# Kernel optimization log

Hardware: AMD Instinct MI355X
Metric: run time of the kernel (lower is better)

Reference implementation:

```python
import jax, jax.numpy as jnp
import numpy as np

D_MODEL = 1024
D_STATE = 16
D_CONV = 4
EXPAND = 2
D_INNER = D_MODEL * EXPAND
BATCH = 4
SEQLEN = 4096


def setup_inputs() -> dict:
    key = jax.random.key(0)
    ks = jax.random.split(key, 10)
    s = 1.0 / np.sqrt(D_MODEL)
    si = 1.0 / np.sqrt(D_INNER)
    return {
        "x": jax.random.normal(ks[0], (BATCH, SEQLEN, D_MODEL), jnp.float32),
        "x_proj_w": jax.random.normal(ks[1], (D_INNER, D_MODEL), jnp.float32) * s,
        "dt_proj_w": jax.random.normal(ks[2], (D_INNER, D_MODEL), jnp.float32) * s,
        "dt_proj_b": jax.random.normal(ks[3], (D_INNER,), jnp.float32) * 0.1,
        "A_log": jax.random.normal(ks[4], (D_INNER, D_STATE), jnp.float32),
        "D": jnp.ones((D_INNER,), jnp.float32),
        "B_proj_w": jax.random.normal(ks[5], (D_STATE, D_MODEL), jnp.float32) * s,
        "C_proj_w": jax.random.normal(ks[6], (D_STATE, D_MODEL), jnp.float32) * s,
        "conv_w": jax.random.normal(ks[7], (D_INNER, 1, D_CONV), jnp.float32) * 0.5,
        "conv_b": jax.random.normal(ks[8], (D_INNER,), jnp.float32) * 0.1,
        "out_proj_w": jax.random.normal(ks[9], (D_MODEL, D_INNER), jnp.float32) * si,
    }


def _selective_scan(xc, delta, A, B, C, D):
    # xc, delta: (b, L, d_inner); B, C: (b, L, d_state); A: (d_inner, d_state)
    batch, seqlen, d_inner = xc.shape
    d_state = A.shape[1]

    def step(h, inp):
        x_t, dt, B_t, C_t = inp  # (b,di), (b,di), (b,ds), (b,ds)
        A_disc = jnp.exp(dt[:, :, None] * A[None])           # (b, di, ds)
        h = A_disc * h + (dt[:, :, None] * B_t[:, None, :]) * x_t[:, :, None]
        y_t = jnp.einsum('bds,bs->bd', h, C_t) + D[None, :] * x_t
        return h, y_t

    h0 = jnp.zeros((batch, d_inner, d_state), xc.dtype)
    xs = (jnp.swapaxes(xc, 0, 1), jnp.swapaxes(delta, 0, 1),
          jnp.swapaxes(B, 0, 1), jnp.swapaxes(C, 0, 1))
    _, ys = jax.lax.scan(step, h0, xs)  # ys: (L, b, d_inner)
    return jnp.swapaxes(ys, 0, 1)


def reference(x, x_proj_w, dt_proj_w, dt_proj_b, A_log, D, B_proj_w, C_proj_w, conv_w, conv_b, out_proj_w):
    seqlen = x.shape[1]
    x_inner = x @ x_proj_w.T  # (b, L, d_inner)
    # causal depthwise conv1d: torch pads both sides by d_conv-1 then keeps first L,
    # equivalent to left-pad (d_conv-1, 0)
    xc = jax.lax.conv_general_dilated(
        jnp.swapaxes(x_inner, 1, 2), conv_w,
        window_strides=(1,), padding=[(D_CONV - 1, 0)],
        dimension_numbers=('NCH', 'OIH', 'NCH'),
        feature_group_count=D_INNER)
    xc = jnp.swapaxes(xc + conv_b[None, :, None], 1, 2)
    xc = jax.nn.silu(xc)
    B = x @ B_proj_w.T
    C = x @ C_proj_w.T
    delta = jax.nn.softplus(x @ dt_proj_w.T + dt_proj_b)
    A = -jnp.exp(A_log.astype(jnp.float32))
    y = _selective_scan(xc, delta, A, B, C, D)
    return y @ out_proj_w.T
```

## Files before the change

### kernel.cpp

```cpp
#include <hip/hip_runtime.h>
#include <hip/hip_bf16.h>
#include <math.h>

typedef __bf16 bf16;
typedef __bf16 bf16x2 __attribute__((ext_vector_type(2)));
typedef __bf16 bf16x8 __attribute__((ext_vector_type(8)));
typedef float f32x4 __attribute__((ext_vector_type(4)));

#define AS_G __attribute__((address_space(1)))
#define AS_L __attribute__((address_space(3)))

__device__ __forceinline__ void async_ld16(const void* g, void* l) {
  __builtin_amdgcn_global_load_lds((const AS_G void*)g, (AS_L void*)l, 16, 0, 0);
}
__device__ __forceinline__ float fexp2(float x) { return __builtin_amdgcn_exp2f(x); }

__global__ void detect_dtype(const void* __restrict__ Dones, int* __restrict__ flag) {
  if (threadIdx.x == 0 && blockIdx.x == 0) {
    *flag = (*(const unsigned int*)Dones == 0x3F803F80u) ? 0 : 1;
  }
}

__global__ __launch_bounds__(256) void to_bf16(
    const void* __restrict__ src, bf16* __restrict__ dst, int n8,
    const int* __restrict__ flag)
{
  const int i = blockIdx.x * 256 + threadIdx.x;
  if (i >= n8) return;
  bf16x8 o;
  if (*flag) {
    const f32x4* s = (const f32x4*)src;
    f32x4 a = s[2*i], b = s[2*i + 1];
    #pragma unroll
    for (int e = 0; e < 4; ++e) { o[e] = (bf16)a[e]; o[e+4] = (bf16)b[e]; }
  } else {
    o = ((const bf16x8*)src)[i];
  }
  ((bf16x8*)dst)[i] = o;
}

template<int EPI>
__global__ __launch_bounds__(256, 2) void gemm_bt(
    const bf16* __restrict__ A, const bf16* __restrict__ W,
    bf16* __restrict__ OutB, float* __restrict__ OutF,
    const bf16* __restrict__ bias, const int* __restrict__ flag,
    int M, int N, int K)
{
  __shared__ bf16 smA[2][128*32];
  __shared__ bf16 smB[2][128*32];
  const int tid  = threadIdx.x;
  const int wave = tid >> 6;
  const int lane = tid & 63;
  const int m0 = blockIdx.x * 128;
  const int n0 = blockIdx.y * 128;
  const int wm = (wave >> 1) * 64;
  const int wn = (wave & 1) * 64;
  const int lm = lane & 15;
  const int q  = lane >> 4;
  const bool f32o = (EPI == 2) && (*flag != 0);

  f32x4 acc[4][4] = {};

  const int chunk0 = wave*128 + lane;
  const int chunk1 = chunk0 + 64;
  const int r0 = chunk0 >> 2, c0 = chunk0 & 3;
  const int r1 = chunk1 >> 2, c1 = chunk1 & 3;
  const int sc0 = c0 ^ ((r0 >> 1) & 3);
  const int sc1 = c1 ^ ((r1 >> 1) & 3);
  const bf16* gA0 = A + (size_t)(m0 + r0)*K + sc0*8;
  const bf16* gA1 = A + (size_t)(m0 + r1)*K + sc1*8;
  const bf16* gB0 = W + (size_t)(n0 + r0)*K + sc0*8;
  const bf16* gB1 = W + (size_t)(n0 + r1)*K + sc1*8;
  const int oA0 = (wave*128     )*8;
  const int oA1 = (wave*128 + 64)*8;

  auto stage = [&](int buf, int k0) {
    async_ld16(gA0 + k0, &smA[buf][oA0]);
    async_ld16(gA1 + k0, &smA[buf][oA1]);
    async_ld16(gB0 + k0, &smB[buf][oA0]);
    async_ld16(gB1 + k0, &smB[buf][oA1]);
  };

  const int sl = (q ^ ((lm >> 1) & 3)) * 8;

  auto compute = [&](const bf16* sA, const bf16* sB) {
    bf16x8 af[4], bfr[4];
    #pragma unroll
    for (int mi = 0; mi < 4; ++mi)
      af[mi] = *(const bf16x8*)(sA + (wm + mi*16 + lm)*32 + sl);
    #pragma unroll
    for (int ni = 0; ni < 4; ++ni)
      bfr[ni] = *(const bf16x8*)(sB + (wn + ni*16 + lm)*32 + sl);
    #pragma unroll
    for (int mi = 0; mi < 4; ++mi)
      #pragma unroll
      for (int ni = 0; ni < 4; ++ni)
        acc[mi][ni] = __builtin_amdgcn_mfma_f32_16x16x32_bf16(af[mi], bfr[ni], acc[mi][ni], 0, 0, 0);
  };

  stage(0, 0);
  __syncthreads();

  for (int k0 = 0; k0 < K; k0 += 64) {
    stage(1, k0 + 32);
    compute(smA[0], smB[0]);
    __syncthreads();
    if (k0 + 64 < K) stage(0, k0 + 64);
    compute(smA[1], smB[1]);
    __syncthreads();
  }

  #pragma unroll
  for (int mi = 0; mi < 4; ++mi) {
    #pragma unroll
    for (int ni = 0; ni < 4; ++ni) {
      const int col = n0 + wn + ni*16 + lm;
      float bval = 0.f;
      if (EPI == 1) bval = (float)bias[col];
      #pragma unroll
      for (int r = 0; r < 4; ++r) {
        const int row = m0 + wm + mi*16 + q*4 + r;
        float v = acc[mi][ni][r];
        if (EPI == 1) {
          v += bval;
          v = (v > 20.f) ? v : __logf(1.f + __expf(v));
        }
        const size_t idx = (size_t)row*N + col;
        if (EPI == 2 && f32o) OutF[idx] = v;
        else                  OutB[idx] = (bf16)v;
      }
    }
  }
}

__global__ __launch_bounds__(64) void bc_gemm(
    const bf16* __restrict__ X,
    const bf16* __restrict__ Bw, const bf16* __restrict__ Cw,
    float* __restrict__ Bout, float* __restrict__ Cout)
{
  const int lane = threadIdx.x;
  const int lm = lane & 15, q = lane >> 4;
  const int m0 = blockIdx.x * 16;
  const bf16* W = blockIdx.y ? Cw : Bw;
  float* O      = blockIdx.y ? Cout : Bout;
  f32x4 acc = {};
  const bf16* pa = X + (size_t)(m0 + lm)*1024 + q*8;
  const bf16* pw = W + (size_t)lm*1024 + q*8;
  for (int k0 = 0; k0 < 1024; k0 += 32) {
    bf16x8 a = *(const bf16x8*)(pa + k0);
    bf16x8 w = *(const bf16x8*)(pw + k0);
    acc = __builtin_amdgcn_mfma_f32_16x16x32_bf16(a, w, acc, 0, 0, 0);
  }
  #pragma unroll
  for (int r = 0; r < 4; ++r)
    O[(size_t)(m0 + q*4 + r)*16 + lm] = acc[r];
}

__global__ __launch_bounds__(256) void conv_silu(
    const bf16* __restrict__ Xin, const bf16* __restrict__ cw,
    const bf16* __restrict__ cb, bf16* __restrict__ Xc)
{
  const int idx = blockIdx.x * 256 + threadIdx.x;
  const int row = idx >> 8;
  const int dv  = (idx & 255) * 8;
  const int t   = row & 4095;
  bf16x8 wv[4];
  const bf16x8* pw = (const bf16x8*)(cw + (size_t)dv*4);
  #pragma unroll
  for (int j = 0; j < 4; ++j) wv[j] = pw[j];
  bf16x8 bv = *(const bf16x8*)(cb + dv);
  float acc[8];
  #pragma unroll
  for (int e = 0; e < 8; ++e) acc[e] = (float)bv[e];
  #pragma unroll
  for (int j = 0; j < 4; ++j) {
    const int tr = t - 3 + j;
    if (tr < 0) continue;
    bf16x8 xv = *(const bf16x8*)(Xin + (size_t)(row - 3 + j)*2048 + dv);
    #pragma unroll
    for (int e = 0; e < 8; ++e) {
      const int li = e*4 + j;
      acc[e] += (float)xv[e] * (float)wv[li >> 3][li & 7];
    }
  }
  bf16x8 o;
  #pragma unroll
  for (int e = 0; e < 8; ++e) {
    float v = acc[e];
    v = v / (1.f + __expf(-v));
    o[e] = (bf16)v;
  }
  *(bf16x8*)(Xc + (size_t)row*2048 + dv) = o;
}

__global__ __launch_bounds__(256) void scan_phase1(
    const bf16* __restrict__ Xc, const bf16* __restrict__ Dt,
    const float* __restrict__ Bm, const bf16* __restrict__ A_log,
    float* __restrict__ Hend, float* __restrict__ Dtsum)
{
  const int tid = threadIdx.x;
  const int d0 = blockIdx.x * 512 + tid * 2;
  const int c = blockIdx.y;
  const int b = blockIdx.z;
  const int t0 = c * 128;
  __shared__ float sB[128*16];
  {
    const f32x4* src = (const f32x4*)(Bm + ((size_t)b*4096 + t0)*16);
    f32x4* dst = (f32x4*)sB;
    dst[tid]       = src[tid];
    dst[tid + 256] = src[tid + 256];
  }
  __syncthreads();
  float A2[2][16];
  #pragma unroll
  for (int u = 0; u < 2; ++u)
    #pragma unroll
    for (int s = 0; s < 16; ++s)
      A2[u][s] = -__expf((float)A_log[(d0+u)*16 + s]) * 1.44269504088896f;
  float h[2][16] = {};
  float dts[2] = {0.f, 0.f};
  const bf16* pX = Xc + ((size_t)b*4096 + t0)*2048 + d0;
  const bf16* pD = Dt + ((size_t)b*4096 + t0)*2048 + d0;
  bf16x2 vD = *(const bf16x2*)pD;
  bf16x2 vX = *(const bf16x2*)pX;
  for (int t = 0; t < 128; ++t) {
    bf16x2 nD = vD, nX = vX;
    if (t < 127) {
      nD = *(const bf16x2*)(pD + (size_t)(t+1)*2048);
      nX = *(const bf16x2*)(pX + (size_t)(t+1)*2048);
    }
    f32x4 Bv[4];
    #pragma unroll
    for (int i = 0; i < 4; ++i) Bv[i] = ((const f32x4*)(sB + t*16))[i];
    #pragma unroll
    for (int u = 0; u < 2; ++u) {
      const float dt = (float)vD[u];
      const float xv = (float)vX[u];
      dts[u] += dt;
      const float dx = dt * xv;
      #pragma unroll
      for (int s = 0; s < 16; ++s) {
        const float ad = fexp2(dt * A2[u][s]);
        h[u][s] = ad*h[u][s] + dx * Bv[s>>2][s&3];
      }
    }
    vD = nD; vX = nX;
  }
  #pragma unroll
  for (int u = 0; u < 2; ++u) {
    const size_t base = (((size_t)b*32 + c)*2048 + d0 + u)*16;
    #pragma unroll
    for (int s = 0; s < 16; ++s) Hend[base + s] = h[u][s];
    Dtsum[((size_t)b*32 + c)*2048 + d0 + u] = dts[u];
  }
}

__global__ __launch_bounds__(256) void scan_phase2(
    float* __restrict__ H,
    const float* __restrict__ Dtsum,
    const bf16* __restrict__ A_log)
{
  const int idx = blockIdx.x*256 + threadIdx.x;
  const int s = idx & 15;
  const int d = (idx >> 4) & 2047;
  const int b = idx >> 15;
  const float A2 = -__expf((float)A_log[d*16 + s]) * 1.44269504088896f;
  float h = 0.f;
  for (int c = 0; c < 32; ++c) {
    const size_t off = (((size_t)b*32 + c)*2048 + d)*16 + s;
    const float hend = H[off];
    H[off] = h;
    const float ap = fexp2(A2 * Dtsum[((size_t)b*32 + c)*2048 + d]);
    h = h*ap + hend;
  }
}

__global__ __launch_bounds__(256) void scan_phase3(
    const bf16* __restrict__ Xc, const bf16* __restrict__ Dt,
    const float* __restrict__ Bm, const float* __restrict__ Cm,
    const bf16* __restrict__ A_log, const bf16* __restrict__ Dvec,
    const float* __restrict__ Hstart, bf16* __restrict__ Y)
{
  const int tid = threadIdx.x;
  const int d0 = blockIdx.x * 512 + tid * 2;
  const int c = blockIdx.y;
  const int b = blockIdx.z;
  const int t0 = c * 128;
  __shared__ float sB[128*16];
  __shared__ float sC[128*16];
  {
    const f32x4* srcB = (const f32x4*)(Bm + ((size_t)b*4096 + t0)*16);
    const f32x4* srcC = (const f32x4*)(Cm + ((size_t)b*4096 + t0)*16);
    ((f32x4*)sB)[tid]       = srcB[tid];
    ((f32x4*)sB)[tid + 256] = srcB[tid + 256];
    ((f32x4*)sC)[tid]       = srcC[tid];
    ((f32x4*)sC)[tid + 256] = srcC[tid + 256];
  }
  __syncthreads();
  float A2[2][16];
  #pragma unroll
  for (int u = 0; u < 2; ++u)
    #pragma unroll
    for (int s = 0; s < 16; ++s)
      A2[u][s] = -__expf((float)A_log[(d0+u)*16 + s]) * 1.44269504088896f;
  float h[2][16];
  #pragma unroll
  for (int u = 0; u < 2; ++u) {
    const size_t base = (((size_t)b*32 + c)*2048 + d0 + u)*16;
    #pragma unroll
    for (int s = 0; s < 16; ++s) h[u][s] = Hstart[base + s];
  }
  const float Dd0 = (float)Dvec[d0];
  const float Dd1 = (float)Dvec[d0 + 1];
  const bf16* pX = Xc + ((size_t)b*4096 + t0)*2048 + d0;
  const bf16* pD = Dt + ((size_t)b*4096 + t0)*2048 + d0;
  bf16*       pY = Y  + ((size_t)b*4096 + t0)*2048 + d0;
  bf16x2 vD = *(const bf16x2*)pD;
  bf16x2 vX = *(const bf16x2*)pX;
  for (int t = 0; t < 128; ++t) {
    bf16x2 nD = vD, nX = vX;
    if (t < 127) {
      nD = *(const bf16x2*)(pD + (size_t)(t+1)*2048);
      nX = *(const bf16x2*)(pX + (size_t)(t+1)*2048);
    }
    f32x4 Bv[4], Cv[4];
    #pragma unroll
    for (int i = 0; i < 4; ++i) {
      Bv[i] = ((const f32x4*)(sB + t*16))[i];
      Cv[i] = ((const f32x4*)(sC + t*16))[i];
    }
    float y[2];
    #pragma unroll
    for (int u = 0; u < 2; ++u) {
      const float dt = (float)vD[u];
      const float xv = (float)vX[u];
      const float dx = dt * xv;
      y[u] = (u ? Dd1 : Dd0) * xv;
      #pragma unroll
      for (int s = 0; s < 16; ++s) {
        const float ad = fexp2(dt * A2[u][s]);
        h[u][s] = ad*h[u][s] + dx * Bv[s>>2][s&3];
        y[u] += h[u][s] * Cv[s>>2][s&3];
      }
    }
    bf16x2 yo; yo[0] = (bf16)y[0]; yo[1] = (bf16)y[1];
    *(bf16x2*)(pY + (size_t)t*2048) = yo;
    vD = nD; vX = nX;
  }
}

extern "C" void kernel_launch(void* const* d_in, const int* in_sizes, int n_in,
                              void* d_out, int out_size, void* d_ws, size_t ws_size,
                              hipStream_t stream)
{
  char* ws = (char*)d_ws;
  size_t off = 0;
  auto alloc = [&](size_t bytes) -> char* {
    char* p = ws + off; off += (bytes + 255) & ~(size_t)255; return p;
  };
  bf16*  xin = (bf16*) alloc((size_t)16384*2048*2);
  bf16*  dlt = (bf16*) alloc((size_t)16384*2048*2);
  bf16*  xc  = (bf16*) alloc((size_t)16384*2048*2);
  float* Bm  = (float*)alloc((size_t)16384*16*4);
  float* Cm  = (float*)alloc((size_t)16384*16*4);
  float* Hst = (float*)alloc((size_t)4*32*2048*16*4);
  float* Dts = (float*)alloc((size_t)4*32*2048*4);
  int*   flag = (int*) alloc(256);
  const int ncanon = 11;
  static const int canon_n[11] = {
    4*4096*1024, 2048*1024, 2048*1024, 2048, 2048*16, 2048,
    16*1024, 16*1024, 2048*4, 2048, 1024*2048 };
  bf16* canon[11];
  for (int i = 0; i < ncanon; ++i) canon[i] = (bf16*)alloc((size_t)canon_n[i]*2);
  if (off > ws_size) return;

  detect_dtype<<<1, 64, 0, stream>>>(d_in[5], flag);
  for (int i = 0; i < ncanon; ++i) {
    const int n8 = canon_n[i] / 8;
    to_bf16<<<(n8 + 255)/256, 256, 0, stream>>>(d_in[i], canon[i], n8, flag);
  }
  const bf16* x          = canon[0];
  const bf16* x_proj_w   = canon[1];
  const bf16* dt_proj_w  = canon[2];
  const bf16* dt_proj_b  = canon[3];
  const bf16* A_log      = canon[4];
  const bf16* Dvec       = canon[5];
  const bf16* B_proj_w   = canon[6];
  const bf16* C_proj_w   = canon[7];
  const bf16* conv_w     = canon[8];
  const bf16* conv_b     = canon[9];
  const bf16* out_proj_w = canon[10];

  gemm_bt<0><<<dim3(128,16), 256, 0, stream>>>(x, x_proj_w,  xin, nullptr, nullptr,   flag, 16384, 2048, 1024);
  gemm_bt<1><<<dim3(128,16), 256, 0, stream>>>(x, dt_proj_w, dlt, nullptr, dt_proj_b, flag, 16384, 2048, 1024);
  bc_gemm<<<dim3(1024,2), 64, 0, stream>>>(x, B_proj_w, C_proj_w, Bm, Cm);
  conv_silu<<<dim3(16384), 256, 0, stream>>>(xin, conv_w, conv_b, xc);
  scan_phase1<<<dim3(4,32,4), 256, 0, stream>>>(xc, dlt, Bm, A_log, Hst, Dts);
  scan_phase2<<<dim3(512),    256, 0, stream>>>(Hst, Dts, A_log);
  scan_phase3<<<dim3(4,32,4), 256, 0, stream>>>(xc, dlt, Bm, Cm, A_log, Dvec, Hst, xin );
  gemm_bt<2><<<dim3(128,8), 256, 0, stream>>>(xin, out_proj_w, (bf16*)d_out, (float*)d_out, nullptr, flag, 16384, 1024, 2048);
}
```

Before: 661.6 us.

## Double scan chunk count to 64 and split y accumulation chains

Shrinks the chunked selective-scan chunk length from 128 to 64 steps, doubling the number of blocks in phases 1 and 3 to expose more parallelism across CUs. Phase 2's sequential carry pass gets twice as many steps. A_log is loaded with vector loads, and the C-dot accumulation in phase 3 is split into four partial sums to shorten the dependency chain. The larger chunk-state buffers are aliased onto the dead x and x_proj_w canonical buffers to avoid extra workspace.

```diff
diff --git a/kernel.cpp b/kernel.cpp
--- a/kernel.cpp
+++ b/kernel.cpp
@@ -9,6 +9,9 @@
 
 #define AS_G __attribute__((address_space(1)))
 #define AS_L __attribute__((address_space(3)))
+
+#define NCHUNK 64
+#define CLEN   64
 
 __device__ __forceinline__ void async_ld16(const void* g, void* l) {
   __builtin_amdgcn_global_load_lds((const AS_G void*)g, (AS_L void*)l, 16, 0, 0);
@@ -202,30 +205,36 @@
   const int d0 = blockIdx.x * 512 + tid * 2;
   const int c = blockIdx.y;
   const int b = blockIdx.z;
-  const int t0 = c * 128;
-  __shared__ float sB[128*16];
+  const int t0 = c * CLEN;
+  __shared__ float sB[CLEN*16];
   {
     const f32x4* src = (const f32x4*)(Bm + ((size_t)b*4096 + t0)*16);
-    f32x4* dst = (f32x4*)sB;
-    dst[tid]       = src[tid];
-    dst[tid + 256] = src[tid + 256];
+    ((f32x4*)sB)[tid] = src[tid];
   }
   __syncthreads();
   float A2[2][16];
-  #pragma unroll
-  for (int u = 0; u < 2; ++u)
-    #pragma unroll
-    for (int s = 0; s < 16; ++s)
-      A2[u][s] = -__expf((float)A_log[(d0+u)*16 + s]) * 1.44269504088896f;
+  {
+    bf16x8 av[4];
+    const bf16x8* pA = (const bf16x8*)(A_log + (size_t)d0*16);
+    #pragma unroll
+    for (int j = 0; j < 4; ++j) av[j] = pA[j];
+    #pragma unroll
+    for (int u = 0; u < 2; ++u)
+      #pragma unroll
+      for (int s = 0; s < 16; ++s) {
+        const int li = u*16 + s;
+        A2[u][s] = -__expf((float)av[li >> 3][li & 7]) * 1.44269504088896f;
+      }
+  }
   float h[2][16] = {};
   float dts[2] = {0.f, 0.f};
   const bf16* pX = Xc + ((size_t)b*4096 + t0)*2048 + d0;
   const bf16* pD = Dt + ((size_t)b*4096 + t0)*2048 + d0;
   bf16x2 vD = *(const bf16x2*)pD;
   bf16x2 vX = *(const bf16x2*)pX;
-  for (int t = 0; t < 128; ++t) {
+  for (int t = 0; t < CLEN; ++t) {
     bf16x2 nD = vD, nX = vX;
-    if (t < 127) {
+    if (t < CLEN-1) {
       nD = *(const bf16x2*)(pD + (size_t)(t+1)*2048);
       nX = *(const bf16x2*)(pX + (size_t)(t+1)*2048);
     }
@@ -248,10 +257,10 @@
   }
   #pragma unroll
   for (int u = 0; u < 2; ++u) {
-    const size_t base = (((size_t)b*32 + c)*2048 + d0 + u)*16;
+    const size_t base = (((size_t)b*NCHUNK + c)*2048 + d0 + u)*16;
     #pragma unroll
     for (int s = 0; s < 16; ++s) Hend[base + s] = h[u][s];
-    Dtsum[((size_t)b*32 + c)*2048 + d0 + u] = dts[u];
+    Dtsum[((size_t)b*NCHUNK + c)*2048 + d0 + u] = dts[u];
   }
 }
 
@@ -266,11 +275,11 @@
   const int b = idx >> 15;
   const float A2 = -__expf((float)A_log[d*16 + s]) * 1.44269504088896f;
   float h = 0.f;
-  for (int c = 0; c < 32; ++c) {
-    const size_t off = (((size_t)b*32 + c)*2048 + d)*16 + s;
+  for (int c = 0; c < NCHUNK; ++c) {
+    const size_t off = (((size_t)b*NCHUNK + c)*2048 + d)*16 + s;
     const float hend = H[off];
     H[off] = h;
-    const float ap = fexp2(A2 * Dtsum[((size_t)b*32 + c)*2048 + d]);
+    const float ap = fexp2(A2 * Dtsum[((size_t)b*NCHUNK + c)*2048 + d]);
     h = h*ap + hend;
   }
 }
@@ -285,28 +294,34 @@
   const int d0 = blockIdx.x * 512 + tid * 2;
   const int c = blockIdx.y;
   const int b = blockIdx.z;
-  const int t0 = c * 128;
-  __shared__ float sB[128*16];
-  __shared__ float sC[128*16];
+  const int t0 = c * CLEN;
+  __shared__ float sB[CLEN*16];
+  __shared__ float sC[CLEN*16];
   {
     const f32x4* srcB = (const f32x4*)(Bm + ((size_t)b*4096 + t0)*16);
     const f32x4* srcC = (const f32x4*)(Cm + ((size_t)b*4096 + t0)*16);
-    ((f32x4*)sB)[tid]       = srcB[tid];
-    ((f32x4*)sB)[tid + 256] = srcB[tid + 256];
-    ((f32x4*)sC)[tid]       = srcC[tid];
-    ((f32x4*)sC)[tid + 256] = srcC[tid + 256];
+    ((f32x4*)sB)[tid] = srcB[tid];
+    ((f32x4*)sC)[tid] = srcC[tid];
   }
   __syncthreads();
   float A2[2][16];
-  #pragma unroll
-  for (int u = 0; u < 2; ++u)
-    #pragma unroll
-    for (int s = 0; s < 16; ++s)
-      A2[u][s] = -__expf((float)A_log[(d0+u)*16 + s]) * 1.44269504088896f;
+  {
+    bf16x8 av[4];
+    const bf16x8* pA = (const bf16x8*)(A_log + (size_t)d0*16);
+    #pragma unroll
+    for (int j = 0; j < 4; ++j) av[j] = pA[j];
+    #pragma unroll
+    for (int u = 0; u < 2; ++u)
+      #pragma unroll
+      for (int s = 0; s < 16; ++s) {
+        const int li = u*16 + s;
+        A2[u][s] = -__expf((float)av[li >> 3][li & 7]) * 1.44269504088896f;
+      }
+  }
   float h[2][16];
   #pragma unroll
   for (int u = 0; u < 2; ++u) {
-    const size_t base = (((size_t)b*32 + c)*2048 + d0 + u)*16;
+    const size_t base = (((size_t)b*NCHUNK + c)*2048 + d0 + u)*16;
     #pragma unroll
     for (int s = 0; s < 16; ++s) h[u][s] = Hstart[base + s];
   }
@@ -317,9 +332,9 @@
   bf16*       pY = Y  + ((size_t)b*4096 + t0)*2048 + d0;
   bf16x2 vD = *(const bf16x2*)pD;
   bf16x2 vX = *(const bf16x2*)pX;
-  for (int t = 0; t < 128; ++t) {
+  for (int t = 0; t < CLEN; ++t) {
     bf16x2 nD = vD, nX = vX;
-    if (t < 127) {
+    if (t < CLEN-1) {
       nD = *(const bf16x2*)(pD + (size_t)(t+1)*2048);
       nX = *(const bf16x2*)(pX + (size_t)(t+1)*2048);
     }
@@ -335,13 +350,14 @@
       const float dt = (float)vD[u];
       const float xv = (float)vX[u];
       const float dx = dt * xv;
-      y[u] = (u ? Dd1 : Dd0) * xv;
+      float yp[4] = {0.f, 0.f, 0.f, 0.f};
       #pragma unroll
       for (int s = 0; s < 16; ++s) {
         const float ad = fexp2(dt * A2[u][s]);
         h[u][s] = ad*h[u][s] + dx * Bv[s>>2][s&3];
-        y[u] += h[u][s] * Cv[s>>2][s&3];
+        yp[s & 3] += h[u][s] * Cv[s>>2][s&3];
       }
+      y[u] = ((yp[0] + yp[1]) + (yp[2] + yp[3])) + (u ? Dd1 : Dd0) * xv;
     }
     bf16x2 yo; yo[0] = (bf16)y[0]; yo[1] = (bf16)y[1];
     *(bf16x2*)(pY + (size_t)t*2048) = yo;
@@ -363,8 +379,6 @@
   bf16*  xc  = (bf16*) alloc((size_t)16384*2048*2);
   float* Bm  = (float*)alloc((size_t)16384*16*4);
   float* Cm  = (float*)alloc((size_t)16384*16*4);
-  float* Hst = (float*)alloc((size_t)4*32*2048*16*4);
-  float* Dts = (float*)alloc((size_t)4*32*2048*4);
   int*   flag = (int*) alloc(256);
   const int ncanon = 11;
   static const int canon_n[11] = {
@@ -372,6 +386,8 @@
     16*1024, 16*1024, 2048*4, 2048, 1024*2048 };
   bf16* canon[11];
   for (int i = 0; i < ncanon; ++i) canon[i] = (bf16*)alloc((size_t)canon_n[i]*2);
+  float* Hst = (float*)canon[0];
+  float* Dts = (float*)canon[1];
   if (off > ws_size) return;
 
   detect_dtype<<<1, 64, 0, stream>>>(d_in[5], flag);
@@ -395,8 +411,8 @@
   gemm_bt<1><<<dim3(128,16), 256, 0, stream>>>(x, dt_proj_w, dlt, nullptr, dt_proj_b, flag, 16384, 2048, 1024);
   bc_gemm<<<dim3(1024,2), 64, 0, stream>>>(x, B_proj_w, C_proj_w, Bm, Cm);
   conv_silu<<<dim3(16384), 256, 0, stream>>>(xin, conv_w, conv_b, xc);
-  scan_phase1<<<dim3(4,32,4), 256, 0, stream>>>(xc, dlt, Bm, A_log, Hst, Dts);
-  scan_phase2<<<dim3(512),    256, 0, stream>>>(Hst, Dts, A_log);
-  scan_phase3<<<dim3(4,32,4), 256, 0, stream>>>(xc, dlt, Bm, Cm, A_log, Dvec, Hst, xin );
+  scan_phase1<<<dim3(4,NCHUNK,4), 256, 0, stream>>>(xc, dlt, Bm, A_log, Hst, Dts);
+  scan_phase2<<<dim3(512),        256, 0, stream>>>(Hst, Dts, A_log);
+  scan_phase3<<<dim3(4,NCHUNK,4), 256, 0, stream>>>(xc, dlt, Bm, Cm, A_log, Dvec, Hst, xin );
   gemm_bt<2><<<dim3(128,8), 256, 0, stream>>>(xin, out_proj_w, (bf16*)d_out, (float*)d_out, nullptr, flag, 16384, 1024, 2048);
 }
```

New measurement: 658.3 us. No clear change (-0.5%).
